# Kernel tuning notes

Hardware: AMD Instinct MI355X
Metric: run time of the kernel (lower is better)

Reference implementation:

```python
import jax, jax.numpy as jnp
import numpy as np
from jax import lax

F = 64          # nb_filters
K_DOWN = 4      # size_kernel_sample
K_RES = 3       # size_kernel_res
DIL = 3         # rate_dilation_res
N_DOWN = 3      # downsampling blocks (one level)
N_RES = 4       # residual sub-blocks per block
N_EMB = 512     # codebook size
BETA = 0.25


def conv1d(x, w, b, stride=1, dil=1, act=True):
    # x: (B,T,C), w: (K,Cin,Cout)
    y = lax.conv_general_dilated(x, w, (stride,), 'SAME', rhs_dilation=(dil,),
                                 dimension_numbers=('NWC', 'WIO', 'NWC')) + b
    return jax.nn.relu(y) if act else y


def conv1d_t(x, w, b, stride):
    # transposed conv, w: (K, Cin, Cout)
    y = lax.conv_transpose(x, w, (stride,), 'SAME',
                           dimension_numbers=('NWC', 'WIO', 'NWC')) + b
    return jax.nn.relu(y)


def setup_inputs() -> dict:
    key = jax.random.key(0)
    ks = jax.random.split(key, 12)
    s_in = 1.0 / np.sqrt(K_DOWN * 1)
    s_f = 1.0 / np.sqrt(K_DOWN * F)
    s_r = 1.0 / np.sqrt(K_RES * F)
    return {
        'x': jax.random.normal(ks[0], (4, 65536, 1), dtype=jnp.float32),
        'w_down0': jax.random.normal(ks[1], (K_DOWN, 1, F), dtype=jnp.float32) * s_in,
        'b_down0': jnp.zeros((F,), jnp.float32),
        'w_down': jax.random.normal(ks[2], (N_DOWN - 1, K_DOWN, F, F), dtype=jnp.float32) * s_f,
        'b_down': jnp.zeros((N_DOWN - 1, F), jnp.float32),
        'w_res_enc': jax.random.normal(ks[3], (N_DOWN, N_RES, 2, K_RES, F, F), dtype=jnp.float32) * s_r,
        'b_res_enc': jnp.zeros((N_DOWN, N_RES, 2, F), jnp.float32),
        'codebook': jax.random.normal(ks[4], (N_EMB, F), dtype=jnp.float32),
        'w_res_dec': jax.random.normal(ks[5], (N_DOWN, N_RES, 2, K_RES, F, F), dtype=jnp.float32) * s_r,
        'b_res_dec': jnp.zeros((N_DOWN, N_RES, 2, F), jnp.float32),
        'w_up': jax.random.normal(ks[6], (N_DOWN, K_DOWN, F, F), dtype=jnp.float32) * s_f,
        'b_up': jnp.zeros((N_DOWN, F), jnp.float32),
        'w_proj': jax.random.normal(ks[7], (K_RES, F, 1), dtype=jnp.float32) * s_r,
        'b_proj': jnp.zeros((1,), jnp.float32),
    }


def reference(x, w_down0, b_down0, w_down, b_down, w_res_enc, b_res_enc,
              codebook, w_res_dec, b_res_dec, w_up, b_up, w_proj, b_proj):
    # ---- Encoder: N_DOWN stride-2 downsampling blocks, each followed by
    # N_RES ForwardResidualSubBlocks (dilated conv -> conv, residual add) ----
    h = conv1d(x, w_down0, b_down0, stride=2)
    for blk in range(N_DOWN):
        if blk > 0:
            h = conv1d(h, w_down[blk - 1], b_down[blk - 1], stride=2)
        for r in range(N_RES):
            y = conv1d(h, w_res_enc[blk, r, 0], b_res_enc[blk, r, 0], dil=DIL)
            y = conv1d(y, w_res_enc[blk, r, 1], b_res_enc[blk, r, 1], dil=1)
            h = h + y
    z_e = h  # (B, T/8, F)

    # ---- VectorQuantiser over channel axis ----
    dot = jnp.einsum('btd,kd->btk', z_e, codebook)          # tensordot
    nz = jnp.sum(jnp.square(z_e), axis=-1, keepdims=True)   # (B,T,1)
    ne = jnp.sum(jnp.square(codebook), axis=-1)             # (K,)
    dist = -2.0 * dot + nz + ne                             # squared cdist
    ids = jnp.argmin(dist, axis=-1)                         # (B,T)
    z_q = codebook[ids]                                     # embedding_lookup
    loss_commit = jnp.mean(jnp.linalg.norm(lax.stop_gradient(z_e) - z_q, axis=-1))
    loss_codebook = jnp.mean(jnp.linalg.norm(z_e - lax.stop_gradient(z_q), axis=-1))
    loss_vq = loss_codebook + BETA * loss_commit
    similarity = dot / jnp.sqrt(nz) / jnp.sqrt(ne)

    # ---- Decoder: residual blocks then stride-2 transposed conv, x N_DOWN ----
    h = z_q
    for blk in range(N_DOWN):
        for r in range(N_RES):
            y = conv1d(h, w_res_dec[blk, r, 0], b_res_dec[blk, r, 0], dil=1)
            y = conv1d(y, w_res_dec[blk, r, 1], b_res_dec[blk, r, 1], dil=DIL)
            h = h + y
        h = conv1d_t(h, w_up[blk], b_up[blk], stride=2)
    x_hat = conv1d(h, w_proj, b_proj, act=False)  # linear projection
    return x_hat, loss_vq, ids, similarity
```

## Files before the change

kernel.cpp:

```cpp
#include <hip/hip_runtime.h>
#include <cstdint>


#define OFF_LOSS 262144
#define OFF_IDS  262145
#define OFF_SIM  294913

__global__ __launch_bounds__(256) void down0_kernel(
    const float* __restrict__ x, const float* __restrict__ w,
    const float* __restrict__ bias, float* __restrict__ y)
{
  int idx = blockIdx.x * 256 + threadIdx.x;
  int co = idx & 63;
  int r  = idx >> 6;
  int t  = r & 32767;
  int b  = r >> 15;
  const float* xb = x + (size_t)b * 65536;
  float acc = bias[co];
  #pragma unroll
  for (int k = 0; k < 4; ++k) {
    int gt = 2 * t - 1 + k;
    float xv = ((unsigned)gt < 65536u) ? xb[gt] : 0.f;
    acc += xv * w[k * 64 + co];
  }
  y[(size_t)idx] = fmaxf(acc, 0.f);
}

template <int DIL, bool HAS_RES, int TT>
__global__ __launch_bounds__(512, 8) void conv3_kernel(
    const float* __restrict__ x, const float* __restrict__ w,
    const float* __restrict__ bias, const float* res,
    float* y, int T)
{
  constexpr int TPL = TT / 64;
  constexpr int XT  = TT + 2 * DIL;
  constexpr int XS  = ((XT - 1) | 15) + 1;
  constexpr int NV  = TPL + 2 * DIL;
  __shared__ float xs[64 * XS];
  const int tid  = threadIdx.x;
  const int lane = tid & 63;
  const int b    = blockIdx.y;
  const int t0   = blockIdx.x * TT;
  const int wv   = __builtin_amdgcn_readfirstlane(tid >> 6);
  const int co0  = __builtin_amdgcn_readfirstlane(wv * 8);

  const float* xb = x + (size_t)b * T * 64;
  for (int e = tid; e < 16 * XT; e += 512) {
    int tl = e >> 4, cq = (e & 15) * 4;
    int cs = tl ^ (((cq >> 2) & 7) << 1);
    int gt = t0 - DIL + tl;
    float4 v = make_float4(0.f, 0.f, 0.f, 0.f);
    if ((unsigned)gt < (unsigned)T) v = *(const float4*)&xb[(size_t)gt * 64 + cq];
    xs[(cq + 0) * XS + cs] = v.x;
    xs[(cq + 1) * XS + cs] = v.y;
    xs[(cq + 2) * XS + cs] = v.z;
    xs[(cq + 3) * XS + cs] = v.w;
  }
  __syncthreads();

  float acc[TPL][8] = {};
  const float* wb = w + co0;
  const int tb = TPL * lane;
  for (int ci = 0; ci < 64; ++ci) {
    const int swz = ((ci >> 2) & 7) << 1;
    const float* xr = xs + ci * XS;
    float xv[NV];
    if constexpr (TPL == 2) {
      #pragma unroll
      for (int q = 0; q < NV / 2; ++q) {
        float2 v = *(const float2*)&xr[(tb + 2 * q) ^ swz];
        xv[2*q] = v.x; xv[2*q+1] = v.y;
      }
    } else {
      #pragma unroll
      for (int j = 0; j < NV; ++j) xv[j] = xr[(tb + j) ^ swz];
    }
    const float* w0 = wb + (0 * 64 + ci) * 64;
    const float* w1 = wb + (1 * 64 + ci) * 64;
    const float* w2 = wb + (2 * 64 + ci) * 64;
    #pragma unroll
    for (int j = 0; j < 8; ++j) {
      float c0 = w0[j], c1 = w1[j], c2 = w2[j];
      #pragma unroll
      for (int i = 0; i < TPL; ++i)
        acc[i][j] = fmaf(xv[i], c0, fmaf(xv[i + DIL], c1, fmaf(xv[i + 2 * DIL], c2, acc[i][j])));
    }
  }

  float bs[8];
  #pragma unroll
  for (int j = 0; j < 8; ++j) bs[j] = bias[co0 + j];
  #pragma unroll
  for (int i = 0; i < TPL; ++i) {
    size_t o = ((size_t)b * T + t0 + tb + i) * 64 + co0;
    float r[8];
    #pragma unroll
    for (int j = 0; j < 8; ++j) r[j] = fmaxf(acc[i][j] + bs[j], 0.f);
    if (HAS_RES) {
      float4 v0 = *(const float4*)&res[o];
      float4 v1 = *(const float4*)&res[o + 4];
      r[0] += v0.x; r[1] += v0.y; r[2] += v0.z; r[3] += v0.w;
      r[4] += v1.x; r[5] += v1.y; r[6] += v1.z; r[7] += v1.w;
    }
    *(float4*)&y[o]     = make_float4(r[0], r[1], r[2], r[3]);
    *(float4*)&y[o + 4] = make_float4(r[4], r[5], r[6], r[7]);
  }
}

__global__ __launch_bounds__(512, 8) void down2_kernel(
    const float* __restrict__ x, const float* __restrict__ w,
    const float* __restrict__ bias, float* __restrict__ y, int Tin)
{
  constexpr int XT = 130, XS = 144;
  __shared__ float xs[64 * XS];
  const int tid  = threadIdx.x;
  const int lane = tid & 63;
  const int b    = blockIdx.y;
  const int t0   = blockIdx.x * 64;
  const int Tout = Tin >> 1;
  const int wv   = __builtin_amdgcn_readfirstlane(tid >> 6);
  const int co0  = __builtin_amdgcn_readfirstlane(wv * 8);

  const float* xb = x + (size_t)b * Tin * 64;
  for (int e = tid; e < 16 * XT; e += 512) {
    int tl = e >> 4, cq = (e & 15) * 4;
    int cs = tl ^ (((cq >> 2) & 7) << 1);
    int gt = 2 * t0 - 1 + tl;
    float4 v = make_float4(0.f, 0.f, 0.f, 0.f);
    if ((unsigned)gt < (unsigned)Tin) v = *(const float4*)&xb[(size_t)gt * 64 + cq];
    xs[(cq + 0) * XS + cs] = v.x;
    xs[(cq + 1) * XS + cs] = v.y;
    xs[(cq + 2) * XS + cs] = v.z;
    xs[(cq + 3) * XS + cs] = v.w;
  }
  __syncthreads();

  float acc[8] = {};
  const float* wb = w + co0;
  for (int ci = 0; ci < 64; ++ci) {
    const int swz = ((ci >> 2) & 7) << 1;
    const float* xr = xs + ci * XS;
    float2 v0 = *(const float2*)&xr[(2 * lane) ^ swz];
    float2 v1 = *(const float2*)&xr[(2 * lane + 2) ^ swz];
    float a0 = v0.x, a1 = v0.y, a2 = v1.x, a3 = v1.y;
    const float* w0 = wb + (0 * 64 + ci) * 64;
    const float* w1 = wb + (1 * 64 + ci) * 64;
    const float* w2 = wb + (2 * 64 + ci) * 64;
    const float* w3 = wb + (3 * 64 + ci) * 64;
    #pragma unroll
    for (int j = 0; j < 8; ++j)
      acc[j] = fmaf(a0, w0[j], fmaf(a1, w1[j], fmaf(a2, w2[j], fmaf(a3, w3[j], acc[j]))));
  }

  size_t o = ((size_t)b * Tout + t0 + lane) * 64 + co0;
  #pragma unroll
  for (int q = 0; q < 2; ++q) {
    float4 rr;
    rr.x = fmaxf(acc[4*q+0] + bias[co0 + 4*q+0], 0.f);
    rr.y = fmaxf(acc[4*q+1] + bias[co0 + 4*q+1], 0.f);
    rr.z = fmaxf(acc[4*q+2] + bias[co0 + 4*q+2], 0.f);
    rr.w = fmaxf(acc[4*q+3] + bias[co0 + 4*q+3], 0.f);
    *(float4*)&y[o + 4 * q] = rr;
  }
}

__global__ __launch_bounds__(512, 8) void up_kernel(
    const float* __restrict__ x, const float* __restrict__ w,
    const float* __restrict__ bias, float* __restrict__ y, int Tin)
{
  constexpr int XT = 66, XS = 80;
  __shared__ float xs[64 * XS];
  const int tid  = threadIdx.x;
  const int lane = tid & 63;
  const int b    = blockIdx.y;
  const int u0   = blockIdx.x * 64;
  const int Tout = Tin << 1;
  const int wv   = __builtin_amdgcn_readfirstlane(tid >> 6);
  const int co0  = __builtin_amdgcn_readfirstlane(wv * 8);

  const float* xb = x + (size_t)b * Tin * 64;
  for (int e = tid; e < 16 * XT; e += 512) {
    int ul = e >> 4, cq = (e & 15) * 4;
    int cs = ul ^ (((cq >> 2) & 7) << 1);
    int gu = u0 - 1 + ul;
    float4 v = make_float4(0.f, 0.f, 0.f, 0.f);
    if ((unsigned)gu < (unsigned)Tin) v = *(const float4*)&xb[(size_t)gu * 64 + cq];
    xs[(cq + 0) * XS + cs] = v.x;
    xs[(cq + 1) * XS + cs] = v.y;
    xs[(cq + 2) * XS + cs] = v.z;
    xs[(cq + 3) * XS + cs] = v.w;
  }
  __syncthreads();

  float acce[8] = {}, acco[8] = {};
  const float* wb = w + co0;
  for (int ci = 0; ci < 64; ++ci) {
    const int swz = ((ci >> 2) & 7) << 1;
    const float* xr = xs + ci * XS;
    float a0 = xr[(lane) ^ swz];
    float a1 = xr[(lane + 1) ^ swz];
    float a2 = xr[(lane + 2) ^ swz];
    const float* w0 = wb + (0 * 64 + ci) * 64;
    const float* w1 = wb + (1 * 64 + ci) * 64;
    const float* w2 = wb + (2 * 64 + ci) * 64;
    const float* w3 = wb + (3 * 64 + ci) * 64;
    #pragma unroll
    for (int j = 0; j < 8; ++j) {
      acce[j] = fmaf(a0, w0[j], fmaf(a1, w2[j], acce[j]));
      acco[j] = fmaf(a1, w1[j], fmaf(a2, w3[j], acco[j]));
    }
  }

  size_t oe = ((size_t)b * Tout + 2 * (u0 + lane)) * 64 + co0;
  size_t oo = oe + 64;
  #pragma unroll
  for (int q = 0; q < 2; ++q) {
    float4 re, ro;
    re.x = fmaxf(acce[4*q+0] + bias[co0 + 4*q+0], 0.f);
    re.y = fmaxf(acce[4*q+1] + bias[co0 + 4*q+1], 0.f);
    re.z = fmaxf(acce[4*q+2] + bias[co0 + 4*q+2], 0.f);
    re.w = fmaxf(acce[4*q+3] + bias[co0 + 4*q+3], 0.f);
    ro.x = fmaxf(acco[4*q+0] + bias[co0 + 4*q+0], 0.f);
    ro.y = fmaxf(acco[4*q+1] + bias[co0 + 4*q+1], 0.f);
    ro.z = fmaxf(acco[4*q+2] + bias[co0 + 4*q+2], 0.f);
    ro.w = fmaxf(acco[4*q+3] + bias[co0 + 4*q+3], 0.f);
    *(float4*)&y[oe + 4 * q] = re;
    *(float4*)&y[oo + 4 * q] = ro;
  }
}

__global__ __launch_bounds__(256) void proj_kernel(
    const float* __restrict__ x, const float* __restrict__ w,
    const float* __restrict__ bias, float* __restrict__ out)
{
  const int lane = threadIdx.x & 63;
  const int wid  = (blockIdx.x * 256 + threadIdx.x) >> 6;
  const float w0 = w[lane], w1 = w[64 + lane], w2 = w[128 + lane];
  const float bb = bias[0];
  size_t base = (size_t)wid * 64;
  for (int i = 0; i < 64; ++i) {
    size_t tau = base + i;
    int b = (int)(tau >> 16);
    int t = (int)(tau & 65535);
    const float* xb = x + ((size_t)b * 65536) * 64;
    float pm = (t > 0)     ? xb[(size_t)(t - 1) * 64 + lane] : 0.f;
    float pc =               xb[(size_t)t * 64 + lane];
    float pp = (t < 65535) ? xb[(size_t)(t + 1) * 64 + lane] : 0.f;
    float s = pm * w0 + pc * w1 + pp * w2;
    #pragma unroll
    for (int off = 32; off; off >>= 1) s += __shfl_down(s, off);
    if (lane == 0) out[tau] = s + bb;
  }
}

__global__ __launch_bounds__(256) void nz_kernel(
    const float* __restrict__ ze, float* __restrict__ nz)
{
  int lane = threadIdx.x & 63;
  int tok  = (blockIdx.x * 256 + threadIdx.x) >> 6;
  float v = ze[(size_t)tok * 64 + lane];
  float s = v * v;
  #pragma unroll
  for (int off = 32; off; off >>= 1) s += __shfl_down(s, off);
  if (lane == 0) nz[tok] = s;
}

__global__ __launch_bounds__(256) void ne_kernel(
    const float* __restrict__ cb, float* __restrict__ ne)
{
  int c = blockIdx.x * 256 + threadIdx.x;
  const float4* p = (const float4*)(cb + (size_t)c * 64);
  float s = 0.f;
  #pragma unroll
  for (int q = 0; q < 16; ++q) {
    float4 v = p[q];
    s += v.x * v.x + v.y * v.y + v.z * v.z + v.w * v.w;
  }
  ne[c] = s;
}

__global__ __launch_bounds__(256) void vq_dots_kernel(
    const float* __restrict__ ze, const float* __restrict__ cb,
    const float* __restrict__ nzbuf, const float* __restrict__ nebuf,
    float* __restrict__ sim_out, float2* __restrict__ pmin)
{
  constexpr int ZS = 68, CS = 132;
  __shared__ float zt[64 * ZS];
  __shared__ float ct[64 * CS];
  const int tid = threadIdx.x;
  const int tx  = tid & 15;
  const int ty  = tid >> 4;
  const int bx  = blockIdx.x, by = blockIdx.y;

  {
    const float* zb = ze + (size_t)bx * 64 * 64;
    #pragma unroll
    for (int it = 0; it < 4; ++it) {
      int e = tid + it * 256;
      int tl = e >> 4, cq = (e & 15) * 4;
      int cs = tl ^ (((cq >> 2) & 7) << 2);
      float4 v = *(const float4*)&zb[tl * 64 + cq];
      zt[(cq + 0) * ZS + cs] = v.x;
      zt[(cq + 1) * ZS + cs] = v.y;
      zt[(cq + 2) * ZS + cs] = v.z;
      zt[(cq + 3) * ZS + cs] = v.w;
    }
    const float* cbb = cb + (size_t)by * 128 * 64;
    #pragma unroll
    for (int it = 0; it < 8; ++it) {
      int e = tid + it * 256;
      int el = e >> 4, cq = (e & 15) * 4;
      int cs = el ^ (((cq >> 2) & 7) << 2);
      float4 v = *(const float4*)&cbb[el * 64 + cq];
      ct[(cq + 0) * CS + cs] = v.x;
      ct[(cq + 1) * CS + cs] = v.y;
      ct[(cq + 2) * CS + cs] = v.z;
      ct[(cq + 3) * CS + cs] = v.w;
    }
  }
  __syncthreads();

  float acc[4][8] = {};
  #pragma unroll 4
  for (int k = 0; k < 64; ++k) {
    const int swz = ((k >> 2) & 7) << 2;
    float4 zv = *(const float4*)&zt[k * ZS + ((ty * 4) ^ swz)];
    float4 c0 = *(const float4*)&ct[k * CS + ((tx * 8) ^ swz)];
    float4 c1 = *(const float4*)&ct[k * CS + ((tx * 8 + 4) ^ swz)];
    float zr[4] = {zv.x, zv.y, zv.z, zv.w};
    float cr[8] = {c0.x, c0.y, c0.z, c0.w, c1.x, c1.y, c1.z, c1.w};
    #pragma unroll
    for (int i = 0; i < 4; ++i)
      #pragma unroll
      for (int j = 0; j < 8; ++j)
        acc[i][j] = fmaf(zr[i], cr[j], acc[i][j]);
  }

  float4 nzq = *(const float4*)&nzbuf[bx * 64 + ty * 4];
  float nzv[4] = {nzq.x, nzq.y, nzq.z, nzq.w};
  float4 ne0  = *(const float4*)&nebuf[by * 128 + tx * 8];
  float4 ne1  = *(const float4*)&nebuf[by * 128 + tx * 8 + 4];
  float nev[8]  = {ne0.x, ne0.y, ne0.z, ne0.w, ne1.x, ne1.y, ne1.z, ne1.w};
  float rsne[8];
  #pragma unroll
  for (int j = 0; j < 8; ++j) rsne[j] = 1.f / sqrtf(nev[j]);
  const int ent0 = by * 128 + tx * 8;

  #pragma unroll
  for (int i = 0; i < 4; ++i) {
    const int tok = bx * 64 + ty * 4 + i;
    const float rsnz = 1.f / sqrtf(nzv[i]);
    float dist[8], simv[8];
    #pragma unroll
    for (int j = 0; j < 8; ++j) {
      dist[j] = (-2.f * acc[i][j] + nzv[i]) + nev[j];
      simv[j] = acc[i][j] * rsnz * rsne[j];
    }
    float* so = sim_out + (size_t)tok * 512 + ent0;
    *(float4*)&so[0] = make_float4(simv[0], simv[1], simv[2], simv[3]);
    *(float4*)&so[4] = make_float4(simv[4], simv[5], simv[6], simv[7]);

    float md = dist[0]; int mi = ent0;
    #pragma unroll
    for (int j = 1; j < 8; ++j)
      if (dist[j] < md) { md = dist[j]; mi = ent0 + j; }
    #pragma unroll
    for (int off = 1; off < 16; off <<= 1) {
      float od = __shfl_xor(md, off);
      int   oi = __shfl_xor(mi, off);
      if (od < md || (od == md && oi < mi)) { md = od; mi = oi; }
    }
    if (tx == 0) pmin[tok * 4 + by] = make_float2(md, (float)mi);
  }
}

__global__ __launch_bounds__(256) void vq_finish_kernel(
    const float* __restrict__ ze, const float* __restrict__ cb,
    const float2* __restrict__ pmin, float* __restrict__ zq,
    float* __restrict__ ids_out, float* __restrict__ blocksum)
{
  const int tid = threadIdx.x;
  const int lane = tid & 63, wvid = tid >> 6;
  float lloss = 0.f;
  for (int it = 0; it < 16; ++it) {
    const int tok = blockIdx.x * 64 + wvid * 16 + it;
    float bd = 1e30f; int bi = 0;
    #pragma unroll
    for (int p = 0; p < 4; ++p) {
      float2 pr = pmin[tok * 4 + p];
      float d = pr.x; int i = (int)pr.y;
      if (d < bd || (d == bd && i < bi)) { bd = d; bi = i; }
    }
    float zev = ze[(size_t)tok * 64 + lane];
    float cv  = cb[(size_t)bi * 64 + lane];
    float df = zev - cv;
    float s = df * df;
    #pragma unroll
    for (int off = 32; off; off >>= 1) s += __shfl_down(s, off);
    zq[(size_t)tok * 64 + lane] = cv;
    if (lane == 0) { ids_out[tok] = (float)bi; lloss += sqrtf(s); }
  }
  __shared__ float ls[4];
  if (lane == 0) ls[wvid] = lloss;
  __syncthreads();
  if (tid == 0) blocksum[blockIdx.x] = ls[0] + ls[1] + ls[2] + ls[3];
}

__global__ void loss_fin_kernel(const float* __restrict__ blocksum,
                                float* __restrict__ out)
{
  const int lane = threadIdx.x;
  float s = 0.f;
  for (int i = lane; i < 512; i += 64) s += blocksum[i];
  #pragma unroll
  for (int off = 32; off; off >>= 1) s += __shfl_down(s, off);
  if (lane == 0) out[0] = 1.25f * s / 32768.f;
}

#define LAUNCH_CONV3(DILV, RESV, XP, WP, BP, RP, YP)                           \
  do {                                                                         \
    if (T >= 16384)                                                            \
      conv3_kernel<DILV, RESV, 128><<<dim3(T / 128, 4), 512, 0, stream>>>(     \
          XP, WP, BP, RP, YP, T);                                              \
    else                                                                       \
      conv3_kernel<DILV, RESV, 64><<<dim3(T / 64, 4), 512, 0, stream>>>(       \
          XP, WP, BP, RP, YP, T);                                              \
  } while (0)

extern "C" void kernel_launch(void* const* d_in, const int* in_sizes, int n_in,
                              void* d_out, int out_size, void* d_ws, size_t ws_size,
                              hipStream_t stream)
{
  const float* x       = (const float*)d_in[0];
  const float* w_down0 = (const float*)d_in[1];
  const float* b_down0 = (const float*)d_in[2];
  const float* w_down  = (const float*)d_in[3];
  const float* b_down  = (const float*)d_in[4];
  const float* w_res_e = (const float*)d_in[5];
  const float* b_res_e = (const float*)d_in[6];
  const float* cb      = (const float*)d_in[7];
  const float* w_res_d = (const float*)d_in[8];
  const float* b_res_d = (const float*)d_in[9];
  const float* w_up    = (const float*)d_in[10];
  const float* b_up    = (const float*)d_in[11];
  const float* w_proj  = (const float*)d_in[12];
  const float* b_proj  = (const float*)d_in[13];

  float* out = (float*)d_out;
  const size_t BUF = (size_t)4 * 65536 * 64;
  float*  bufA     = (float*)d_ws;
  float*  bufB     = bufA + BUF;
  float*  nzbuf    = bufB + BUF;
  float*  nebuf    = nzbuf + 32768;
  float2* pmin     = (float2*)(nebuf + 512);
  float*  blocksum = (float*)(pmin + 32768 * 4);

  float* h = bufA;
  float* tmp = bufB;

  down0_kernel<<<32768, 256, 0, stream>>>(x, w_down0, b_down0, h);
  int T = 32768;
  for (int blk = 0; blk < 3; ++blk) {
    if (blk > 0) {
      down2_kernel<<<dim3(T / 2 / 64, 4), 512, 0, stream>>>(
          h, w_down + (size_t)(blk - 1) * 4 * 64 * 64, b_down + (blk - 1) * 64, tmp, T);
      T >>= 1;
      float* s = h; h = tmp; tmp = s;
    }
    for (int r = 0; r < 4; ++r) {
      const float* w0p = w_res_e + (((size_t)blk * 4 + r) * 2 + 0) * 3 * 64 * 64;
      const float* w1p = w_res_e + (((size_t)blk * 4 + r) * 2 + 1) * 3 * 64 * 64;
      const float* b0p = b_res_e + (((size_t)blk * 4 + r) * 2 + 0) * 64;
      const float* b1p = b_res_e + (((size_t)blk * 4 + r) * 2 + 1) * 64;
      LAUNCH_CONV3(3, false, h, w0p, b0p, nullptr, tmp);
      LAUNCH_CONV3(1, true,  tmp, w1p, b1p, h, h);
    }
  }

  nz_kernel<<<8192, 256, 0, stream>>>(h, nzbuf);
  ne_kernel<<<2, 256, 0, stream>>>(cb, nebuf);
  vq_dots_kernel<<<dim3(512, 4), 256, 0, stream>>>(h, cb, nzbuf, nebuf, out + OFF_SIM, pmin);
  vq_finish_kernel<<<512, 256, 0, stream>>>(h, cb, pmin, tmp, out + OFF_IDS, blocksum);
  loss_fin_kernel<<<1, 64, 0, stream>>>(blocksum, out + OFF_LOSS);
  { float* s = h; h = tmp; tmp = s; }

  for (int blk = 0; blk < 3; ++blk) {
    for (int r = 0; r < 4; ++r) {
      const float* w0p = w_res_d + (((size_t)blk * 4 + r) * 2 + 0) * 3 * 64 * 64;
      const float* w1p = w_res_d + (((size_t)blk * 4 + r) * 2 + 1) * 3 * 64 * 64;
      const float* b0p = b_res_d + (((size_t)blk * 4 + r) * 2 + 0) * 64;
      const float* b1p = b_res_d + (((size_t)blk * 4 + r) * 2 + 1) * 64;
      LAUNCH_CONV3(1, false, h, w0p, b0p, nullptr, tmp);
      LAUNCH_CONV3(3, true,  tmp, w1p, b1p, h, h);
    }
    up_kernel<<<dim3(2 * T / 128, 4), 512, 0, stream>>>(
        h, w_up + (size_t)blk * 4 * 64 * 64, b_up + blk * 64, tmp, T);
    T <<= 1;
    float* s = h; h = tmp; tmp = s;
  }

  proj_kernel<<<1024, 256, 0, stream>>>(h, w_proj, b_proj, out);
}
```

Measured before the change: 1.607 ms.

## Restructure transposed-conv kernel: lane per output channel, 16 time steps per thread

```diff
diff --git a/kernel.cpp b/kernel.cpp
--- a/kernel.cpp
+++ b/kernel.cpp
@@ -164,24 +164,23 @@
   }
 }
 
-__global__ __launch_bounds__(512, 8) void up_kernel(
+__global__ __launch_bounds__(512, 4) void up_kernel(
     const float* __restrict__ x, const float* __restrict__ w,
     const float* __restrict__ bias, float* __restrict__ y, int Tin)
 {
-  constexpr int XT = 66, XS = 80;
+  constexpr int XT = 130, XS = 160;
   __shared__ float xs[64 * XS];
   const int tid  = threadIdx.x;
   const int lane = tid & 63;
+  const int wv   = tid >> 6;
   const int b    = blockIdx.y;
-  const int u0   = blockIdx.x * 64;
+  const int u0   = blockIdx.x * 128;
   const int Tout = Tin << 1;
-  const int wv   = __builtin_amdgcn_readfirstlane(tid >> 6);
-  const int co0  = __builtin_amdgcn_readfirstlane(wv * 8);
 
   const float* xb = x + (size_t)b * Tin * 64;
   for (int e = tid; e < 16 * XT; e += 512) {
     int ul = e >> 4, cq = (e & 15) * 4;
-    int cs = ul ^ (((cq >> 2) & 7) << 1);
+    int cs = ul ^ (((cq >> 2) & 7) << 2);
     int gu = u0 - 1 + ul;
     float4 v = make_float4(0.f, 0.f, 0.f, 0.f);
     if ((unsigned)gu < (unsigned)Tin) v = *(const float4*)&xb[(size_t)gu * 64 + cq];
@@ -192,40 +191,45 @@
   }
   __syncthreads();
 
-  float acce[8] = {}, acco[8] = {};
-  const float* wb = w + co0;
-  for (int ci = 0; ci < 64; ++ci) {
-    const int swz = ((ci >> 2) & 7) << 1;
-    const float* xr = xs + ci * XS;
-    float a0 = xr[(lane) ^ swz];
-    float a1 = xr[(lane + 1) ^ swz];
-    float a2 = xr[(lane + 2) ^ swz];
-    const float* w0 = wb + (0 * 64 + ci) * 64;
-    const float* w1 = wb + (1 * 64 + ci) * 64;
-    const float* w2 = wb + (2 * 64 + ci) * 64;
-    const float* w3 = wb + (3 * 64 + ci) * 64;
-    #pragma unroll
-    for (int j = 0; j < 8; ++j) {
-      acce[j] = fmaf(a0, w0[j], fmaf(a1, w2[j], acce[j]));
-      acco[j] = fmaf(a1, w1[j], fmaf(a2, w3[j], acco[j]));
-    }
-  }
-
-  size_t oe = ((size_t)b * Tout + 2 * (u0 + lane)) * 64 + co0;
-  size_t oo = oe + 64;
-  #pragma unroll
-  for (int q = 0; q < 2; ++q) {
-    float4 re, ro;
-    re.x = fmaxf(acce[4*q+0] + bias[co0 + 4*q+0], 0.f);
-    re.y = fmaxf(acce[4*q+1] + bias[co0 + 4*q+1], 0.f);
-    re.z = fmaxf(acce[4*q+2] + bias[co0 + 4*q+2], 0.f);
-    re.w = fmaxf(acce[4*q+3] + bias[co0 + 4*q+3], 0.f);
-    ro.x = fmaxf(acco[4*q+0] + bias[co0 + 4*q+0], 0.f);
-    ro.y = fmaxf(acco[4*q+1] + bias[co0 + 4*q+1], 0.f);
-    ro.z = fmaxf(acco[4*q+2] + bias[co0 + 4*q+2], 0.f);
-    ro.w = fmaxf(acco[4*q+3] + bias[co0 + 4*q+3], 0.f);
-    *(float4*)&y[oe + 4 * q] = re;
-    *(float4*)&y[oo + 4 * q] = ro;
+  const int tb = wv * 16;
+  float acce[16] = {}, acco[16] = {};
+  const float* wbase = w + lane;
+
+  for (int cb = 0; cb < 64; cb += 8) {
+    float wt0[8], wt1[8], wt2[8], wt3[8];
+    #pragma unroll
+    for (int i = 0; i < 8; ++i) {
+      wt0[i] = wbase[(0 * 64 + cb + i) * 64];
+      wt1[i] = wbase[(1 * 64 + cb + i) * 64];
+      wt2[i] = wbase[(2 * 64 + cb + i) * 64];
+      wt3[i] = wbase[(3 * 64 + cb + i) * 64];
+    }
+    #pragma unroll
+    for (int i = 0; i < 8; ++i) {
+      const int ci  = cb + i;
+      const int swz = ((ci >> 2) & 7) << 2;
+      const float* xr = xs + ci * XS;
+      float xq[20];
+      #pragma unroll
+      for (int q = 0; q < 5; ++q) {
+        float4 v = *(const float4*)&xr[(tb + 4 * q) ^ swz];
+        xq[4*q+0] = v.x; xq[4*q+1] = v.y; xq[4*q+2] = v.z; xq[4*q+3] = v.w;
+      }
+      #pragma unroll
+      for (int u = 0; u < 16; ++u) {
+        acce[u] = fmaf(xq[u],     wt0[i], fmaf(xq[u + 1], wt2[i], acce[u]));
+        acco[u] = fmaf(xq[u + 1], wt1[i], fmaf(xq[u + 2], wt3[i], acco[u]));
+      }
+    }
+  }
+
+  const float bb = bias[lane];
+  #pragma unroll
+  for (int u = 0; u < 16; ++u) {
+    const size_t p = (size_t)(u0 + tb + u);
+    size_t oe = ((size_t)b * Tout + 2 * p) * 64 + lane;
+    y[oe]      = fmaxf(acce[u] + bb, 0.f);
+    y[oe + 64] = fmaxf(acco[u] + bb, 0.f);
   }
 }
 
@@ -493,7 +497,7 @@
       LAUNCH_CONV3(1, false, h, w0p, b0p, nullptr, tmp);
       LAUNCH_CONV3(3, true,  tmp, w1p, b1p, h, h);
     }
-    up_kernel<<<dim3(2 * T / 128, 4), 512, 0, stream>>>(
+    up_kernel<<<dim3(T / 128, 4), 512, 0, stream>>>(
         h, w_up + (size_t)blk * 4 * 64 * 64, b_up + blk * 64, tmp, T);
     T <<= 1;
     float* s = h; h = tmp; tmp = s;
```

Result: slower. 1.707 ms (+6.2%).

## Split conv3 output channels across grid z and stage weights in LDS

Applied to the files above, without the earlier changes.

```diff
diff --git a/kernel.cpp b/kernel.cpp
--- a/kernel.cpp
+++ b/kernel.cpp
@@ -26,23 +26,26 @@
   y[(size_t)idx] = fmaxf(acc, 0.f);
 }
 
-template <int DIL, bool HAS_RES, int TT>
-__global__ __launch_bounds__(512, 8) void conv3_kernel(
+template <int DIL, bool HAS_RES>
+__global__ __launch_bounds__(512, 4) void conv3_kernel(
     const float* __restrict__ x, const float* __restrict__ w,
     const float* __restrict__ bias, const float* res,
     float* y, int T)
 {
-  constexpr int TPL = TT / 64;
+  constexpr int TT  = 128;
   constexpr int XT  = TT + 2 * DIL;
-  constexpr int XS  = ((XT - 1) | 15) + 1;
-  constexpr int NV  = TPL + 2 * DIL;
+  constexpr int XS  = 144;
+  constexpr int NV  = 2 + 2 * DIL;
   __shared__ float xs[64 * XS];
+  __shared__ float ws[3 * 64 * 32];
   const int tid  = threadIdx.x;
   const int lane = tid & 63;
   const int b    = blockIdx.y;
+  const int z    = blockIdx.z;
   const int t0   = blockIdx.x * TT;
   const int wv   = __builtin_amdgcn_readfirstlane(tid >> 6);
-  const int co0  = __builtin_amdgcn_readfirstlane(wv * 8);
+  const int cl   = __builtin_amdgcn_readfirstlane(wv * 4);
+  const int co0  = z * 32 + cl;
 
   const float* xb = x + (size_t)b * T * 64;
   for (int e = tid; e < 16 * XT; e += 512) {
@@ -56,54 +59,51 @@
     xs[(cq + 2) * XS + cs] = v.z;
     xs[(cq + 3) * XS + cs] = v.w;
   }
+  for (int e = tid; e < 1536; e += 512) {
+    int c = (e & 7) * 4, rr = e >> 3;
+    *(float4*)&ws[rr * 32 + c] = *(const float4*)&w[rr * 64 + z * 32 + c];
+  }
   __syncthreads();
 
-  float acc[TPL][8] = {};
-  const float* wb = w + co0;
-  const int tb = TPL * lane;
+  float acc[2][4] = {};
+  const int tb = 2 * lane;
   for (int ci = 0; ci < 64; ++ci) {
     const int swz = ((ci >> 2) & 7) << 1;
     const float* xr = xs + ci * XS;
     float xv[NV];
-    if constexpr (TPL == 2) {
+    #pragma unroll
+    for (int q = 0; q < NV / 2; ++q) {
+      float2 v = *(const float2*)&xr[(tb + 2 * q) ^ swz];
+      xv[2*q] = v.x; xv[2*q+1] = v.y;
+    }
+    float4 W0 = *(const float4*)&ws[(0 * 64 + ci) * 32 + cl];
+    float4 W1 = *(const float4*)&ws[(1 * 64 + ci) * 32 + cl];
+    float4 W2 = *(const float4*)&ws[(2 * 64 + ci) * 32 + cl];
+    float c0[4] = {W0.x, W0.y, W0.z, W0.w};
+    float c1[4] = {W1.x, W1.y, W1.z, W1.w};
+    float c2[4] = {W2.x, W2.y, W2.z, W2.w};
+    #pragma unroll
+    for (int j = 0; j < 4; ++j) {
       #pragma unroll
-      for (int q = 0; q < NV / 2; ++q) {
-        float2 v = *(const float2*)&xr[(tb + 2 * q) ^ swz];
-        xv[2*q] = v.x; xv[2*q+1] = v.y;
-      }
-    } else {
-      #pragma unroll
-      for (int j = 0; j < NV; ++j) xv[j] = xr[(tb + j) ^ swz];
-    }
-    const float* w0 = wb + (0 * 64 + ci) * 64;
-    const float* w1 = wb + (1 * 64 + ci) * 64;
-    const float* w2 = wb + (2 * 64 + ci) * 64;
-    #pragma unroll
-    for (int j = 0; j < 8; ++j) {
-      float c0 = w0[j], c1 = w1[j], c2 = w2[j];
-      #pragma unroll
-      for (int i = 0; i < TPL; ++i)
-        acc[i][j] = fmaf(xv[i], c0, fmaf(xv[i + DIL], c1, fmaf(xv[i + 2 * DIL], c2, acc[i][j])));
-    }
-  }
-
-  float bs[8];
-  #pragma unroll
-  for (int j = 0; j < 8; ++j) bs[j] = bias[co0 + j];
-  #pragma unroll
-  for (int i = 0; i < TPL; ++i) {
+      for (int i = 0; i < 2; ++i)
+        acc[i][j] = fmaf(xv[i], c0[j], fmaf(xv[i + DIL], c1[j], fmaf(xv[i + 2 * DIL], c2[j], acc[i][j])));
+    }
+  }
+
+  float bs[4];
+  #pragma unroll
+  for (int j = 0; j < 4; ++j) bs[j] = bias[co0 + j];
+  #pragma unroll
+  for (int i = 0; i < 2; ++i) {
     size_t o = ((size_t)b * T + t0 + tb + i) * 64 + co0;
-    float r[8];
-    #pragma unroll
-    for (int j = 0; j < 8; ++j) r[j] = fmaxf(acc[i][j] + bs[j], 0.f);
+    float r[4];
+    #pragma unroll
+    for (int j = 0; j < 4; ++j) r[j] = fmaxf(acc[i][j] + bs[j], 0.f);
     if (HAS_RES) {
       float4 v0 = *(const float4*)&res[o];
-      float4 v1 = *(const float4*)&res[o + 4];
       r[0] += v0.x; r[1] += v0.y; r[2] += v0.z; r[3] += v0.w;
-      r[4] += v1.x; r[5] += v1.y; r[6] += v1.z; r[7] += v1.w;
-    }
-    *(float4*)&y[o]     = make_float4(r[0], r[1], r[2], r[3]);
-    *(float4*)&y[o + 4] = make_float4(r[4], r[5], r[6], r[7]);
+    }
+    *(float4*)&y[o] = make_float4(r[0], r[1], r[2], r[3]);
   }
 }
 
@@ -418,14 +418,8 @@
 }
 
 #define LAUNCH_CONV3(DILV, RESV, XP, WP, BP, RP, YP)                           \
-  do {                                                                         \
-    if (T >= 16384)                                                            \
-      conv3_kernel<DILV, RESV, 128><<<dim3(T / 128, 4), 512, 0, stream>>>(     \
-          XP, WP, BP, RP, YP, T);                                              \
-    else                                                                       \
-      conv3_kernel<DILV, RESV, 64><<<dim3(T / 64, 4), 512, 0, stream>>>(       \
-          XP, WP, BP, RP, YP, T);                                              \
-  } while (0)
+  conv3_kernel<DILV, RESV><<<dim3(T / 128, 4, 2), 512, 0, stream>>>(           \
+      XP, WP, BP, RP, YP, T)
 
 extern "C" void kernel_launch(void* const* d_in, const int* in_sizes, int n_in,
                               void* d_out, int out_size, void* d_ws, size_t ws_size,
```

Measured after the change: 2.039 ms. 26.9% more time.

## Fuse both residual-block convolutions into one kernel with halo recompute

Applied to the files above, without the earlier changes.

```diff
diff --git a/kernel.cpp b/kernel.cpp
--- a/kernel.cpp
+++ b/kernel.cpp
@@ -26,17 +26,18 @@
   y[(size_t)idx] = fmaxf(acc, 0.f);
 }
 
-template <int DIL, bool HAS_RES, int TT>
-__global__ __launch_bounds__(512, 8) void conv3_kernel(
-    const float* __restrict__ x, const float* __restrict__ w,
-    const float* __restrict__ bias, const float* res,
-    float* y, int T)
-{
-  constexpr int TPL = TT / 64;
-  constexpr int XT  = TT + 2 * DIL;
-  constexpr int XS  = ((XT - 1) | 15) + 1;
-  constexpr int NV  = TPL + 2 * DIL;
+template <int DILA, int DILB>
+__global__ __launch_bounds__(512, 8) void resblock_kernel(
+    const float* __restrict__ x, const float* __restrict__ wa,
+    const float* __restrict__ ba, const float* __restrict__ wb,
+    const float* __restrict__ bbv, float* __restrict__ y, int T)
+{
+  constexpr int H  = DILA + DILB;
+  constexpr int TT = 64 - 2 * DILB;
+  constexpr int XT = 64 + 2 * DILA;
+  constexpr int XS = 80;
   __shared__ float xs[64 * XS];
+  __shared__ float is_[64 * 64 + 16];
   const int tid  = threadIdx.x;
   const int lane = tid & 63;
   const int b    = blockIdx.y;
@@ -48,7 +49,7 @@
   for (int e = tid; e < 16 * XT; e += 512) {
     int tl = e >> 4, cq = (e & 15) * 4;
     int cs = tl ^ (((cq >> 2) & 7) << 1);
-    int gt = t0 - DIL + tl;
+    int gt = t0 - H + tl;
     float4 v = make_float4(0.f, 0.f, 0.f, 0.f);
     if ((unsigned)gt < (unsigned)T) v = *(const float4*)&xb[(size_t)gt * 64 + cq];
     xs[(cq + 0) * XS + cs] = v.x;
@@ -58,52 +59,58 @@
   }
   __syncthreads();
 
-  float acc[TPL][8] = {};
-  const float* wb = w + co0;
-  const int tb = TPL * lane;
-  for (int ci = 0; ci < 64; ++ci) {
-    const int swz = ((ci >> 2) & 7) << 1;
-    const float* xr = xs + ci * XS;
-    float xv[NV];
-    if constexpr (TPL == 2) {
+  {
+    const int it = lane;
+    float acc[8] = {};
+    const float* wba = wa + co0;
+    for (int ci = 0; ci < 64; ++ci) {
+      const int swz = ((ci >> 2) & 7) << 1;
+      const float* xr = xs + ci * XS;
+      float x0 = xr[(it) ^ swz];
+      float x1 = xr[(it + DILA) ^ swz];
+      float x2 = xr[(it + 2 * DILA) ^ swz];
+      const float* w0 = wba + (0 * 64 + ci) * 64;
+      const float* w1 = wba + (1 * 64 + ci) * 64;
+      const float* w2 = wba + (2 * 64 + ci) * 64;
       #pragma unroll
-      for (int q = 0; q < NV / 2; ++q) {
-        float2 v = *(const float2*)&xr[(tb + 2 * q) ^ swz];
-        xv[2*q] = v.x; xv[2*q+1] = v.y;
+      for (int j = 0; j < 8; ++j)
+        acc[j] = fmaf(x0, w0[j], fmaf(x1, w1[j], fmaf(x2, w2[j], acc[j])));
+    }
+    const bool valid = (unsigned)(t0 - DILB + it) < (unsigned)T;
+    #pragma unroll
+    for (int j = 0; j < 8; ++j)
+      is_[(co0 + j) * 64 + it] = valid ? fmaxf(acc[j] + ba[co0 + j], 0.f) : 0.f;
+  }
+  __syncthreads();
+
+  {
+    float acc[8] = {};
+    const float* wbb = wb + co0;
+    for (int ci = 0; ci < 64; ++ci) {
+      const float* ir = is_ + ci * 64;
+      float v0 = ir[lane];
+      float v1 = ir[lane + DILB];
+      float v2 = ir[lane + 2 * DILB];
+      const float* w0 = wbb + (0 * 64 + ci) * 64;
+      const float* w1 = wbb + (1 * 64 + ci) * 64;
+      const float* w2 = wbb + (2 * 64 + ci) * 64;
+      #pragma unroll
+      for (int j = 0; j < 8; ++j)
+        acc[j] = fmaf(v0, w0[j], fmaf(v1, w1[j], fmaf(v2, w2[j], acc[j])));
+    }
+    if (lane < TT && (unsigned)(t0 + lane) < (unsigned)T) {
+      float r[8];
+      #pragma unroll
+      for (int j = 0; j < 8; ++j) {
+        const int row = co0 + j;
+        const int swzj = ((row >> 2) & 7) << 1;
+        float xres = xs[row * XS + ((lane + H) ^ swzj)];
+        r[j] = fmaxf(acc[j] + bbv[row], 0.f) + xres;
       }
-    } else {
-      #pragma unroll
-      for (int j = 0; j < NV; ++j) xv[j] = xr[(tb + j) ^ swz];
-    }
-    const float* w0 = wb + (0 * 64 + ci) * 64;
-    const float* w1 = wb + (1 * 64 + ci) * 64;
-    const float* w2 = wb + (2 * 64 + ci) * 64;
-    #pragma unroll
-    for (int j = 0; j < 8; ++j) {
-      float c0 = w0[j], c1 = w1[j], c2 = w2[j];
-      #pragma unroll
-      for (int i = 0; i < TPL; ++i)
-        acc[i][j] = fmaf(xv[i], c0, fmaf(xv[i + DIL], c1, fmaf(xv[i + 2 * DIL], c2, acc[i][j])));
-    }
-  }
-
-  float bs[8];
-  #pragma unroll
-  for (int j = 0; j < 8; ++j) bs[j] = bias[co0 + j];
-  #pragma unroll
-  for (int i = 0; i < TPL; ++i) {
-    size_t o = ((size_t)b * T + t0 + tb + i) * 64 + co0;
-    float r[8];
-    #pragma unroll
-    for (int j = 0; j < 8; ++j) r[j] = fmaxf(acc[i][j] + bs[j], 0.f);
-    if (HAS_RES) {
-      float4 v0 = *(const float4*)&res[o];
-      float4 v1 = *(const float4*)&res[o + 4];
-      r[0] += v0.x; r[1] += v0.y; r[2] += v0.z; r[3] += v0.w;
-      r[4] += v1.x; r[5] += v1.y; r[6] += v1.z; r[7] += v1.w;
-    }
-    *(float4*)&y[o]     = make_float4(r[0], r[1], r[2], r[3]);
-    *(float4*)&y[o + 4] = make_float4(r[4], r[5], r[6], r[7]);
+      size_t o = ((size_t)b * T + t0 + lane) * 64 + co0;
+      *(float4*)&y[o]     = make_float4(r[0], r[1], r[2], r[3]);
+      *(float4*)&y[o + 4] = make_float4(r[4], r[5], r[6], r[7]);
+    }
   }
 }
 
@@ -417,16 +424,6 @@
   if (lane == 0) out[0] = 1.25f * s / 32768.f;
 }
 
-#define LAUNCH_CONV3(DILV, RESV, XP, WP, BP, RP, YP)                           \
-  do {                                                                         \
-    if (T >= 16384)                                                            \
-      conv3_kernel<DILV, RESV, 128><<<dim3(T / 128, 4), 512, 0, stream>>>(     \
-          XP, WP, BP, RP, YP, T);                                              \
-    else                                                                       \
-      conv3_kernel<DILV, RESV, 64><<<dim3(T / 64, 4), 512, 0, stream>>>(       \
-          XP, WP, BP, RP, YP, T);                                              \
-  } while (0)
-
 extern "C" void kernel_launch(void* const* d_in, const int* in_sizes, int n_in,
                               void* d_out, int out_size, void* d_ws, size_t ws_size,
                               hipStream_t stream)
@@ -472,8 +469,9 @@
       const float* w1p = w_res_e + (((size_t)blk * 4 + r) * 2 + 1) * 3 * 64 * 64;
       const float* b0p = b_res_e + (((size_t)blk * 4 + r) * 2 + 0) * 64;
       const float* b1p = b_res_e + (((size_t)blk * 4 + r) * 2 + 1) * 64;
-      LAUNCH_CONV3(3, false, h, w0p, b0p, nullptr, tmp);
-      LAUNCH_CONV3(1, true,  tmp, w1p, b1p, h, h);
+      resblock_kernel<3, 1><<<dim3((T + 61) / 62, 4), 512, 0, stream>>>(
+          h, w0p, b0p, w1p, b1p, tmp, T);
+      float* s = h; h = tmp; tmp = s;
     }
   }
 
@@ -490,8 +488,9 @@
       const float* w1p = w_res_d + (((size_t)blk * 4 + r) * 2 + 1) * 3 * 64 * 64;
       const float* b0p = b_res_d + (((size_t)blk * 4 + r) * 2 + 0) * 64;
       const float* b1p = b_res_d + (((size_t)blk * 4 + r) * 2 + 1) * 64;
-      LAUNCH_CONV3(1, false, h, w0p, b0p, nullptr, tmp);
-      LAUNCH_CONV3(3, true,  tmp, w1p, b1p, h, h);
+      resblock_kernel<1, 3><<<dim3((T + 57) / 58, 4), 512, 0, stream>>>(
+          h, w0p, b0p, w1p, b1p, tmp, T);
+      float* s = h; h = tmp; tmp = s;
     }
     up_kernel<<<dim3(2 * T / 128, 4), 512, 0, stream>>>(
         h, w_up + (size_t)blk * 4 * 64 * 64, b_up + blk * 64, tmp, T);
```

New measurement: 1.754 ms. +9.2%, slower.
